# Performance work log

Hardware: AMD Instinct MI355X
Metric: run time of the kernel (lower is better)

The kernel has to match this reference:

```python
import jax, jax.numpy as jnp
import numpy as np
from math import ceil, log2

LEVELS = 8
# pywt 'db4' filters (length 8)
DB4_DEC_HI = np.array([-0.23037781330885523, 0.7148465705525415, -0.6308807679295904,
                       -0.02798376941698385, 0.18703481171888114, 0.030841381835986965,
                       -0.032883011666982945, -0.010597401784997278], dtype=np.float32)
DB4_REC_HI = np.array([-0.010597401784997278, -0.032883011666982945, 0.030841381835986965,
                       0.18703481171888114, -0.02798376941698385, -0.6308807679295904,
                       0.7148465705525415, -0.23037781330885523], dtype=np.float32)


def setup_inputs() -> dict:
    key = jax.random.key(0)
    x = jax.random.normal(key, (2048, 3000), dtype=jnp.float32)
    scaling = jnp.tile(jnp.asarray(DB4_DEC_HI), (LEVELS, 1))       # [levels, 8]
    scaling_rec = jnp.tile(jnp.asarray(DB4_REC_HI), (LEVELS, 1))   # [levels, 8]
    return {"input": x, "scaling": scaling, "scaling_rec": scaling_rec}


def _make_wavelet(h):
    # g = flip(h); g[1::2] *= -1
    g = jnp.flip(h, axis=-1)
    signs = jnp.where(jnp.arange(g.shape[-1]) % 2 == 1, -1.0, 1.0).astype(g.dtype)
    return g * signs


def _circ_conv(x, filt, transpose=False):
    # FFT-based circular convolution (filter zero-padded to input length)
    L = x.shape[-1]
    ra = jnp.fft.rfft(x)
    rb = jnp.fft.rfft(filt, n=L)
    if transpose:
        rb = jnp.conj(rb)
    return jnp.fft.irfft(ra * rb, n=L)


def _upsample2(x):
    # interleave zeros: out[:, ::2] = x
    n, k = x.shape
    out = jnp.zeros((n, 2 * k), dtype=x.dtype)
    return out.at[:, ::2].set(x)


def _forward(x, scaling, scaling_rec):
    levels = scaling.shape[0]
    m = x.shape[1]
    L = 2 ** ceil(log2(m))
    p0 = (L - m) // 2
    p1 = ceil((L - m) / 2)
    x = jnp.pad(x, ((0, 0), (p0, p1)), mode="edge")  # ReplicationPad1d

    approx = x
    wav_coeffs = []
    for lvl in range(levels):
        wavelet = _make_wavelet(scaling_rec[lvl])
        details = _circ_conv(approx, wavelet)[:, ::2]
        approx = _circ_conv(approx, scaling[lvl])[:, ::2]
        wav_coeffs.append(details)
    wav_coeffs.append(approx)

    # (no thresholding: the original forward copies coeffs unmodified)
    filtered = list(wav_coeffs)
    approx = filtered[-1]
    for lvl in reversed(range(levels)):
        details = filtered[lvl]
        wav_syn = _make_wavelet(scaling_rec[lvl])
        d_rec = _circ_conv(_upsample2(details), wav_syn, transpose=True)
        a_rec = _circ_conv(_upsample2(approx), scaling[lvl], transpose=True)
        approx = d_rec + a_rec

    recon = approx[:, p0:m + p1]
    coeffs = jnp.concatenate(wav_coeffs, axis=-1)  # total length == L
    return recon, coeffs


def reference(input, scaling, scaling_rec):
    return _forward(input, scaling, scaling_rec)
```

## Files before the change

kernel.cpp:

```cpp
#include <hip/hip_runtime.h>

#define NROWS 2048
#define MLEN  3000
#define LPAD  4096
#define PAD0  548
#define NLVL  8
#define NT    512
#define RPB   2

union F4 { float4 v; float f[4]; };

__device__ inline void lds_barrier() {
    asm volatile("s_waitcnt lgkmcnt(0)\n\ts_barrier" ::: "memory");
}

__global__ __launch_bounds__(NT, 8) void despawn_kernel(
    const float* __restrict__ x,
    const float* __restrict__ scaling,
    const float* __restrict__ scaling_rec,
    float* __restrict__ recon_out,
    float* __restrict__ coef_out)
{
    __shared__ __align__(16) float LDSBUF[RPB][4672];

    const int tid = threadIdx.x;
    const int r   = tid >> 8;
    const int t   = tid & 255;
    const int row = blockIdx.x * RPB + r;
    float* const sa = &LDSBUF[r][0];
    float* const sb = &LDSBUF[r][2048];
    float* const cs = &LDSBUF[r][4160];

    float* const crow = coef_out + (size_t)row * LPAD;
    const float* xr = x + (size_t)row * MLEN;

    {
        const int lag = (blockIdx.x >> 3) & 3;
        for (int i = 0; i < lag; ++i) __builtin_amdgcn_s_sleep(8);
    }

    {
        float S[8], Wr[8];
#pragma unroll
        for (int k = 0; k < 8; ++k) { S[k] = scaling[k]; Wr[k] = scaling_rec[7 - k]; }
#pragma unroll
        for (int h = 0; h < 2; ++h) {
            const int j0 = 1024 * h;
            const int n0 = 2 * j0 + 8 * t - 8;
            F4 V0, V1, V2, V3;
            if (n0 >= PAD0 && n0 + 15 <= PAD0 + MLEN - 1) {
                const float4* src = reinterpret_cast<const float4*>(xr + (n0 - PAD0));
                V0.v = src[0]; V1.v = src[1]; V2.v = src[2]; V3.v = src[3];
            } else {
                const float x0  = xr[0];
                const float xhi = xr[MLEN - 1];
#pragma unroll
                for (int j = 0; j < 16; ++j) {
                    const int n = n0 + j;
                    const int m = (n < 0) ? n + LPAD : n;
                    float val;
                    if (m < PAD0)              val = x0;
                    else if (m >= PAD0 + MLEN) val = xhi;
                    else                       val = xr[m - PAD0];
                    if (j < 4)       V0.f[j & 3] = val;
                    else if (j < 8)  V1.f[j & 3] = val;
                    else if (j < 12) V2.f[j & 3] = val;
                    else             V3.f[j & 3] = val;
                }
            }
            float e[8] = {V0.f[0],V0.f[2],V1.f[0],V1.f[2],V2.f[0],V2.f[2],V3.f[0],V3.f[2]};
            float o[8] = {V0.f[1],V0.f[3],V1.f[1],V1.f[3],V2.f[1],V2.f[3],V3.f[1],V3.f[3]};
            float ds[4], as[4];
            __builtin_amdgcn_s_setprio(1);
#pragma unroll
            for (int u = 0; u < 4; ++u) {
                float d = 0.f, a = 0.f;
#pragma unroll
                for (int m = 0; m < 4; ++m) {
                    const float vE = e[4 + u - m];
                    const float vO = o[3 + u - m];
                    d = fmaf(vE, Wr[2 * m], d);
                    d = fmaf(vO, -Wr[2 * m + 1], d);
                    a = fmaf(vE, S[2 * m], a);
                    a = fmaf(vO, S[2 * m + 1], a);
                }
                ds[u] = d; as[u] = a;
            }
            __builtin_amdgcn_s_setprio(0);
            F4 dv; dv.f[0] = ds[0]; dv.f[1] = ds[1]; dv.f[2] = ds[2]; dv.f[3] = ds[3];
            reinterpret_cast<float4*>(crow + j0)[t] = dv.v;
            *reinterpret_cast<float2*>(sa + (j0 >> 1) + 2 * t)        = make_float2(as[0], as[2]);
            *reinterpret_cast<float2*>(sa + 1024 + (j0 >> 1) + 2 * t) = make_float2(as[1], as[3]);
        }
    }
    lds_barrier();

    {
        float* cur = sa;
        float* alt = sb;
        int H = 1024;
        int coff = 2048;
        for (int lvl = 1; lvl < NLVL; ++lvl) {
            float S[8], Wr[8];
#pragma unroll
            for (int k = 0; k < 8; ++k) {
                S[k]  = scaling[lvl * 8 + k];
                Wr[k] = scaling_rec[lvl * 8 + 7 - k];
            }
            const int q = H >> 2;
            const int qm = q - 1;
            const float4* ev4 = reinterpret_cast<const float4*>(cur);
            const float4* od4 = reinterpret_cast<const float4*>(cur + H);
            float4* dst4 = reinterpret_cast<float4*>(crow + coff);
            float4* mir4 = (lvl == 1) ? reinterpret_cast<float4*>(sb + 1088)
                         : (lvl == 2) ? reinterpret_cast<float4*>(sa + 512)
                                      : reinterpret_cast<float4*>(cs + (coff - 3584));
            for (int tt = t; tt < q; tt += 256) {
                F4 Ea, Eb, Oa, Ob;
                Ea.v = ev4[(tt - 1) & qm];
                Eb.v = ev4[tt];
                Oa.v = od4[(tt - 1) & qm];
                Ob.v = od4[tt];
                float e[8] = {Ea.f[0],Ea.f[1],Ea.f[2],Ea.f[3],Eb.f[0],Eb.f[1],Eb.f[2],Eb.f[3]};
                float o[8] = {Oa.f[0],Oa.f[1],Oa.f[2],Oa.f[3],Ob.f[0],Ob.f[1],Ob.f[2],Ob.f[3]};
                float ds[4], as[4];
                __builtin_amdgcn_s_setprio(1);
#pragma unroll
                for (int u = 0; u < 4; ++u) {
                    float d = 0.f, a = 0.f;
#pragma unroll
                    for (int m = 0; m < 4; ++m) {
                        const float vE = e[4 + u - m];
                        const float vO = o[3 + u - m];
                        d = fmaf(vE, Wr[2 * m], d);
                        d = fmaf(vO, -Wr[2 * m + 1], d);
                        a = fmaf(vE, S[2 * m], a);
                        a = fmaf(vO, S[2 * m + 1], a);
                    }
                    ds[u] = d; as[u] = a;
                }
                __builtin_amdgcn_s_setprio(0);
                F4 dv; dv.f[0] = ds[0]; dv.f[1] = ds[1]; dv.f[2] = ds[2]; dv.f[3] = ds[3];
                dst4[tt] = dv.v;
                mir4[tt] = dv.v;
                if (lvl < NLVL - 1) {
                    *reinterpret_cast<float2*>(alt + 2 * tt)            = make_float2(as[0], as[2]);
                    *reinterpret_cast<float2*>(alt + (H >> 1) + 2 * tt) = make_float2(as[1], as[3]);
                } else {
                    F4 av; av.f[0] = as[0]; av.f[1] = as[1]; av.f[2] = as[2]; av.f[3] = as[3];
                    *reinterpret_cast<float4*>(cs + 496 + 4 * tt)         = av.v;
                    *reinterpret_cast<float4*>(crow + LPAD - 16 + 4 * tt) = av.v;
                }
            }
            lds_barrier();
            coff += H;
            float* tmp = cur; cur = alt; alt = tmp;
            H >>= 1;
        }
    }

    __syncthreads();

    const float* a = cs + 496;
    float* obuf = sa;
    int len = 16;
    for (int lvl = NLVL - 1; lvl >= 1; --lvl) {
        float S[8], Wr[8];
#pragma unroll
        for (int k = 0; k < 8; ++k) {
            S[k]  = scaling[lvl * 8 + k];
            Wr[k] = scaling_rec[lvl * 8 + 7 - k];
        }
        const int Mout = len << 1;
        const int doff = LPAD - (LPAD >> lvl);
        const float4* d4 = (lvl >= 3) ? reinterpret_cast<const float4*>(cs + (doff - 3584))
                         : (lvl == 2) ? reinterpret_cast<const float4*>(sa + 512)
                                      : reinterpret_cast<const float4*>(sb + 1088);
        const float4* a4 = reinterpret_cast<const float4*>(a);
        const int gq = Mout >> 3;
        const int fm = (len >> 2) - 1;
        for (int g = t; g < gq; g += 256) {
            F4 Da, Db, Aa, Ab;
            Da.v = d4[g]; Db.v = d4[(g + 1) & fm];
            Aa.v = a4[g]; Ab.v = a4[(g + 1) & fm];
            float dd[8] = {Da.f[0],Da.f[1],Da.f[2],Da.f[3],Db.f[0],Db.f[1],Db.f[2],Db.f[3]};
            float aa[8] = {Aa.f[0],Aa.f[1],Aa.f[2],Aa.f[3],Ab.f[0],Ab.f[1],Ab.f[2],Ab.f[3]};
            float out[8];
            __builtin_amdgcn_s_setprio(1);
#pragma unroll
            for (int u = 0; u < 8; ++u) {
                const int p = u & 1, c = (u + 1) >> 1;
                float s = 0.f;
#pragma unroll
                for (int m = 0; m < 4; ++m) {
                    const float w = Wr[p + 2 * m];
                    s = fmaf(dd[c + m], p ? -w : w, s);
                    s = fmaf(aa[c + m], S[p + 2 * m], s);
                }
                out[u] = s;
            }
            __builtin_amdgcn_s_setprio(0);
            F4 o0, o1;
            o0.f[0] = out[0]; o0.f[1] = out[1]; o0.f[2] = out[2]; o0.f[3] = out[3];
            o1.f[0] = out[4]; o1.f[1] = out[5]; o1.f[2] = out[6]; o1.f[3] = out[7];
            float4* ob4 = reinterpret_cast<float4*>(obuf + 8 * g);
            ob4[0] = o0.v; ob4[1] = o1.v;
        }
        lds_barrier();
        a = obuf;
        obuf = (obuf == sa) ? sb : sa;
        len = Mout;
    }

    {
        float S[8], Wr[8];
#pragma unroll
        for (int k = 0; k < 8; ++k) { S[k] = scaling[k]; Wr[k] = scaling_rec[7 - k]; }
        const float4* d4 = reinterpret_cast<const float4*>(crow);
        const float4* a4 = reinterpret_cast<const float4*>(a);
        const int fm = (len >> 2) - 1;
        float* const ro = recon_out + (size_t)row * MLEN;
        for (int g = t; g < (LPAD >> 3); g += 256) {
            F4 Da, Db, Aa, Ab;
            Da.v = d4[g]; Db.v = d4[(g + 1) & fm];
            Aa.v = a4[g]; Ab.v = a4[(g + 1) & fm];
            float dd[8] = {Da.f[0],Da.f[1],Da.f[2],Da.f[3],Db.f[0],Db.f[1],Db.f[2],Db.f[3]};
            float aa[8] = {Aa.f[0],Aa.f[1],Aa.f[2],Aa.f[3],Ab.f[0],Ab.f[1],Ab.f[2],Ab.f[3]};
            float out[8];
            __builtin_amdgcn_s_setprio(1);
#pragma unroll
            for (int u = 0; u < 8; ++u) {
                const int p = u & 1, c = (u + 1) >> 1;
                float s = 0.f;
#pragma unroll
                for (int m = 0; m < 4; ++m) {
                    const float w = Wr[p + 2 * m];
                    s = fmaf(dd[c + m], p ? -w : w, s);
                    s = fmaf(aa[c + m], S[p + 2 * m], s);
                }
                out[u] = s;
            }
            __builtin_amdgcn_s_setprio(0);
            const int n0 = 8 * g;
            if (n0 >= PAD0 && n0 + 8 <= PAD0 + MLEN) {
                F4 o0, o1;
                o0.f[0] = out[0]; o0.f[1] = out[1]; o0.f[2] = out[2]; o0.f[3] = out[3];
                o1.f[0] = out[4]; o1.f[1] = out[5]; o1.f[2] = out[6]; o1.f[3] = out[7];
                float4* r4 = reinterpret_cast<float4*>(ro + (n0 - PAD0));
                r4[0] = o0.v; r4[1] = o1.v;
            } else {
#pragma unroll
                for (int u = 0; u < 8; ++u) {
                    const int n = n0 + u;
                    if (n >= PAD0 && n < PAD0 + MLEN) ro[n - PAD0] = out[u];
                }
            }
        }
    }
}

extern "C" void kernel_launch(void* const* d_in, const int* in_sizes, int n_in,
                              void* d_out, int out_size, void* d_ws, size_t ws_size,
                              hipStream_t stream) {
    const float* x           = (const float*)d_in[0];
    const float* scaling     = (const float*)d_in[1];
    const float* scaling_rec = (const float*)d_in[2];
    float* recon = (float*)d_out;
    float* coefo = recon + (size_t)NROWS * MLEN;
    despawn_kernel<<<dim3(NROWS / RPB), dim3(NT), 0, stream>>>(x, scaling, scaling_rec,
                                                               recon, coefo);
    (void)in_sizes; (void)n_in; (void)out_size; (void)d_ws; (void)ws_size;
}
```

Before: 95.11 us.

## Run small wavelet levels in a single wave without block barriers

The deep levels (3-7) of the forward transform and the matching inverse levels, where each row has at most 64 active work items, now run inside one wavefront per row. They use only an LDS wait in place of a block-wide s_barrier. The remaining levels are unrolled with constant sizes and strides, which drops the loop and dynamic pointer selection. This removes about ten block barriers per row, in exchange for relying on wave-level ordering of LDS accesses within the 64-lane group.

```diff
diff --git a/kernel.cpp b/kernel.cpp
--- a/kernel.cpp
+++ b/kernel.cpp
@@ -12,6 +12,9 @@
 
 __device__ inline void lds_barrier() {
     asm volatile("s_waitcnt lgkmcnt(0)\n\ts_barrier" ::: "memory");
+}
+__device__ inline void wave_lds_fence() {
+    asm volatile("s_waitcnt lgkmcnt(0)" ::: "memory");
 }
 
 __global__ __launch_bounds__(NT, 8) void despawn_kernel(
@@ -100,7 +103,7 @@
         float* alt = sb;
         int H = 1024;
         int coff = 2048;
-        for (int lvl = 1; lvl < NLVL; ++lvl) {
+        for (int lvl = 1; lvl <= 2; ++lvl) {
             float S[8], Wr[8];
 #pragma unroll
             for (int k = 0; k < 8; ++k) {
@@ -113,9 +116,9 @@
             const float4* od4 = reinterpret_cast<const float4*>(cur + H);
             float4* dst4 = reinterpret_cast<float4*>(crow + coff);
             float4* mir4 = (lvl == 1) ? reinterpret_cast<float4*>(sb + 1088)
-                         : (lvl == 2) ? reinterpret_cast<float4*>(sa + 512)
-                                      : reinterpret_cast<float4*>(cs + (coff - 3584));
-            for (int tt = t; tt < q; tt += 256) {
+                                      : reinterpret_cast<float4*>(sa + 512);
+            if (t < q) {
+                const int tt = t;
                 F4 Ea, Eb, Oa, Ob;
                 Ea.v = ev4[(tt - 1) & qm];
                 Eb.v = ev4[tt];
@@ -143,43 +146,134 @@
                 F4 dv; dv.f[0] = ds[0]; dv.f[1] = ds[1]; dv.f[2] = ds[2]; dv.f[3] = ds[3];
                 dst4[tt] = dv.v;
                 mir4[tt] = dv.v;
-                if (lvl < NLVL - 1) {
-                    *reinterpret_cast<float2*>(alt + 2 * tt)            = make_float2(as[0], as[2]);
-                    *reinterpret_cast<float2*>(alt + (H >> 1) + 2 * tt) = make_float2(as[1], as[3]);
-                } else {
-                    F4 av; av.f[0] = as[0]; av.f[1] = as[1]; av.f[2] = as[2]; av.f[3] = as[3];
-                    *reinterpret_cast<float4*>(cs + 496 + 4 * tt)         = av.v;
-                    *reinterpret_cast<float4*>(crow + LPAD - 16 + 4 * tt) = av.v;
-                }
+                *reinterpret_cast<float2*>(alt + 2 * tt)            = make_float2(as[0], as[2]);
+                *reinterpret_cast<float2*>(alt + (H >> 1) + 2 * tt) = make_float2(as[1], as[3]);
             }
             lds_barrier();
             coff += H;
             float* tmp = cur; cur = alt; alt = tmp;
             H >>= 1;
         }
-    }
-
-    __syncthreads();
-
-    const float* a = cs + 496;
-    float* obuf = sa;
-    int len = 16;
-    for (int lvl = NLVL - 1; lvl >= 1; --lvl) {
+
+        if (t < 64) {
+            for (int lvl = 3; lvl < NLVL; ++lvl) {
+                float S[8], Wr[8];
+#pragma unroll
+                for (int k = 0; k < 8; ++k) {
+                    S[k]  = scaling[lvl * 8 + k];
+                    Wr[k] = scaling_rec[lvl * 8 + 7 - k];
+                }
+                const int q = H >> 2;
+                const int qm = q - 1;
+                const float4* ev4 = reinterpret_cast<const float4*>(cur);
+                const float4* od4 = reinterpret_cast<const float4*>(cur + H);
+                float4* dst4 = reinterpret_cast<float4*>(crow + coff);
+                float4* mir4 = reinterpret_cast<float4*>(cs + (coff - 3584));
+                if (t < q) {
+                    const int tt = t;
+                    F4 Ea, Eb, Oa, Ob;
+                    Ea.v = ev4[(tt - 1) & qm];
+                    Eb.v = ev4[tt];
+                    Oa.v = od4[(tt - 1) & qm];
+                    Ob.v = od4[tt];
+                    float e[8] = {Ea.f[0],Ea.f[1],Ea.f[2],Ea.f[3],Eb.f[0],Eb.f[1],Eb.f[2],Eb.f[3]};
+                    float o[8] = {Oa.f[0],Oa.f[1],Oa.f[2],Oa.f[3],Ob.f[0],Ob.f[1],Ob.f[2],Ob.f[3]};
+                    float ds[4], as[4];
+#pragma unroll
+                    for (int u = 0; u < 4; ++u) {
+                        float d = 0.f, a = 0.f;
+#pragma unroll
+                        for (int m = 0; m < 4; ++m) {
+                            const float vE = e[4 + u - m];
+                            const float vO = o[3 + u - m];
+                            d = fmaf(vE, Wr[2 * m], d);
+                            d = fmaf(vO, -Wr[2 * m + 1], d);
+                            a = fmaf(vE, S[2 * m], a);
+                            a = fmaf(vO, S[2 * m + 1], a);
+                        }
+                        ds[u] = d; as[u] = a;
+                    }
+                    F4 dv; dv.f[0] = ds[0]; dv.f[1] = ds[1]; dv.f[2] = ds[2]; dv.f[3] = ds[3];
+                    dst4[tt] = dv.v;
+                    mir4[tt] = dv.v;
+                    if (lvl < NLVL - 1) {
+                        *reinterpret_cast<float2*>(alt + 2 * tt)            = make_float2(as[0], as[2]);
+                        *reinterpret_cast<float2*>(alt + (H >> 1) + 2 * tt) = make_float2(as[1], as[3]);
+                    } else {
+                        F4 av; av.f[0] = as[0]; av.f[1] = as[1]; av.f[2] = as[2]; av.f[3] = as[3];
+                        *reinterpret_cast<float4*>(cs + 496 + 4 * tt)         = av.v;
+                        *reinterpret_cast<float4*>(crow + LPAD - 16 + 4 * tt) = av.v;
+                    }
+                }
+                wave_lds_fence();
+                coff += H;
+                float* tmp = cur; cur = alt; alt = tmp;
+                H >>= 1;
+            }
+
+            const float* a = cs + 496;
+            float* obuf = sa;
+            int len = 16;
+            for (int lvl = NLVL - 1; lvl >= 3; --lvl) {
+                float S[8], Wr[8];
+#pragma unroll
+                for (int k = 0; k < 8; ++k) {
+                    S[k]  = scaling[lvl * 8 + k];
+                    Wr[k] = scaling_rec[lvl * 8 + 7 - k];
+                }
+                const int Mout = len << 1;
+                const int doff = LPAD - (LPAD >> lvl);
+                const float4* d4 = reinterpret_cast<const float4*>(cs + (doff - 3584));
+                const float4* a4 = reinterpret_cast<const float4*>(a);
+                const int gq = Mout >> 3;
+                const int fm = (len >> 2) - 1;
+                if (t < gq) {
+                    const int g = t;
+                    F4 Da, Db, Aa, Ab;
+                    Da.v = d4[g]; Db.v = d4[(g + 1) & fm];
+                    Aa.v = a4[g]; Ab.v = a4[(g + 1) & fm];
+                    float dd[8] = {Da.f[0],Da.f[1],Da.f[2],Da.f[3],Db.f[0],Db.f[1],Db.f[2],Db.f[3]};
+                    float aa[8] = {Aa.f[0],Aa.f[1],Aa.f[2],Aa.f[3],Ab.f[0],Ab.f[1],Ab.f[2],Ab.f[3]};
+                    float out[8];
+#pragma unroll
+                    for (int u = 0; u < 8; ++u) {
+                        const int p = u & 1, c = (u + 1) >> 1;
+                        float s = 0.f;
+#pragma unroll
+                        for (int m = 0; m < 4; ++m) {
+                            const float w = Wr[p + 2 * m];
+                            s = fmaf(dd[c + m], p ? -w : w, s);
+                            s = fmaf(aa[c + m], S[p + 2 * m], s);
+                        }
+                        out[u] = s;
+                    }
+                    F4 o0, o1;
+                    o0.f[0] = out[0]; o0.f[1] = out[1]; o0.f[2] = out[2]; o0.f[3] = out[3];
+                    o1.f[0] = out[4]; o1.f[1] = out[5]; o1.f[2] = out[6]; o1.f[3] = out[7];
+                    float4* ob4 = reinterpret_cast<float4*>(obuf + 8 * g);
+                    ob4[0] = o0.v; ob4[1] = o1.v;
+                }
+                wave_lds_fence();
+                a = obuf;
+                obuf = (obuf == sa) ? sb : sa;
+                len = Mout;
+            }
+        }
+    }
+    lds_barrier();
+
+    {
         float S[8], Wr[8];
 #pragma unroll
         for (int k = 0; k < 8; ++k) {
-            S[k]  = scaling[lvl * 8 + k];
-            Wr[k] = scaling_rec[lvl * 8 + 7 - k];
-        }
-        const int Mout = len << 1;
-        const int doff = LPAD - (LPAD >> lvl);
-        const float4* d4 = (lvl >= 3) ? reinterpret_cast<const float4*>(cs + (doff - 3584))
-                         : (lvl == 2) ? reinterpret_cast<const float4*>(sa + 512)
-                                      : reinterpret_cast<const float4*>(sb + 1088);
-        const float4* a4 = reinterpret_cast<const float4*>(a);
-        const int gq = Mout >> 3;
-        const int fm = (len >> 2) - 1;
-        for (int g = t; g < gq; g += 256) {
+            S[k]  = scaling[2 * 8 + k];
+            Wr[k] = scaling_rec[2 * 8 + 7 - k];
+        }
+        const float4* d4 = reinterpret_cast<const float4*>(sa + 512);
+        const float4* a4 = reinterpret_cast<const float4*>(sa);
+        const int fm = 127;
+        if (t < 128) {
+            const int g = t;
             F4 Da, Db, Aa, Ab;
             Da.v = d4[g]; Db.v = d4[(g + 1) & fm];
             Aa.v = a4[g]; Ab.v = a4[(g + 1) & fm];
@@ -203,22 +297,60 @@
             F4 o0, o1;
             o0.f[0] = out[0]; o0.f[1] = out[1]; o0.f[2] = out[2]; o0.f[3] = out[3];
             o1.f[0] = out[4]; o1.f[1] = out[5]; o1.f[2] = out[6]; o1.f[3] = out[7];
-            float4* ob4 = reinterpret_cast<float4*>(obuf + 8 * g);
+            float4* ob4 = reinterpret_cast<float4*>(sb + 8 * g);
             ob4[0] = o0.v; ob4[1] = o1.v;
         }
-        lds_barrier();
-        a = obuf;
-        obuf = (obuf == sa) ? sb : sa;
-        len = Mout;
-    }
+    }
+    lds_barrier();
+
+    {
+        float S[8], Wr[8];
+#pragma unroll
+        for (int k = 0; k < 8; ++k) {
+            S[k]  = scaling[1 * 8 + k];
+            Wr[k] = scaling_rec[1 * 8 + 7 - k];
+        }
+        const float4* d4 = reinterpret_cast<const float4*>(sb + 1088);
+        const float4* a4 = reinterpret_cast<const float4*>(sb);
+        const int fm = 255;
+        {
+            const int g = t;
+            F4 Da, Db, Aa, Ab;
+            Da.v = d4[g]; Db.v = d4[(g + 1) & fm];
+            Aa.v = a4[g]; Ab.v = a4[(g + 1) & fm];
+            float dd[8] = {Da.f[0],Da.f[1],Da.f[2],Da.f[3],Db.f[0],Db.f[1],Db.f[2],Db.f[3]};
+            float aa[8] = {Aa.f[0],Aa.f[1],Aa.f[2],Aa.f[3],Ab.f[0],Ab.f[1],Ab.f[2],Ab.f[3]};
+            float out[8];
+            __builtin_amdgcn_s_setprio(1);
+#pragma unroll
+            for (int u = 0; u < 8; ++u) {
+                const int p = u & 1, c = (u + 1) >> 1;
+                float s = 0.f;
+#pragma unroll
+                for (int m = 0; m < 4; ++m) {
+                    const float w = Wr[p + 2 * m];
+                    s = fmaf(dd[c + m], p ? -w : w, s);
+                    s = fmaf(aa[c + m], S[p + 2 * m], s);
+                }
+                out[u] = s;
+            }
+            __builtin_amdgcn_s_setprio(0);
+            F4 o0, o1;
+            o0.f[0] = out[0]; o0.f[1] = out[1]; o0.f[2] = out[2]; o0.f[3] = out[3];
+            o1.f[0] = out[4]; o1.f[1] = out[5]; o1.f[2] = out[6]; o1.f[3] = out[7];
+            float4* ob4 = reinterpret_cast<float4*>(sa + 8 * g);
+            ob4[0] = o0.v; ob4[1] = o1.v;
+        }
+    }
+    asm volatile("s_waitcnt vmcnt(0) lgkmcnt(0)\n\ts_barrier" ::: "memory");
 
     {
         float S[8], Wr[8];
 #pragma unroll
         for (int k = 0; k < 8; ++k) { S[k] = scaling[k]; Wr[k] = scaling_rec[7 - k]; }
         const float4* d4 = reinterpret_cast<const float4*>(crow);
-        const float4* a4 = reinterpret_cast<const float4*>(a);
-        const int fm = (len >> 2) - 1;
+        const float4* a4 = reinterpret_cast<const float4*>(sa);
+        const int fm = 511;
         float* const ro = recon_out + (size_t)row * MLEN;
         for (int g = t; g < (LPAD >> 3); g += 256) {
             F4 Da, Db, Aa, Ab;
```

Result: slower. 97.56 us (+2.6%).
